# Kernel tuning notes

Hardware: AMD Instinct MI355X
Metric: run time of the kernel (lower is better)

Reference implementation:

```python
import jax, jax.numpy as jnp
import numpy as np

INF = 1000000000000.0
B, H, EMB = 64, 512, 512
V = 32000
S_ENC, S_SEQ = 512, 512
ENC2 = 512  # 2 * encoder_hidden_dim
NUM_OOV = 50


def setup_inputs() -> dict:
    key = jax.random.key(0)
    ks = jax.random.split(key, 24)
    s = 0.02
    nrm = lambda k, shp: jax.random.normal(k, shp, jnp.float32) * s
    inp = {}
    inp["input_ids"] = jax.random.randint(ks[0], (B,), 0, V)
    inp["prev_context"] = jax.random.normal(ks[1], (B, H), jnp.float32)
    inp["h0"] = jax.random.normal(ks[2], (1, B, H), jnp.float32)
    inp["c0"] = jax.random.normal(ks[3], (1, B, H), jnp.float32)
    inp["encoder_outputs"] = jax.random.normal(ks[4], (B, S_ENC, H), jnp.float32)
    inp["seqs_encoding"] = jax.random.normal(ks[5], (B, S_SEQ, ENC2), jnp.float32)
    inp["seqs_encoding_mask"] = jax.random.randint(ks[6], (B, S_SEQ), 0, 2).astype(bool)
    ext = jax.random.randint(ks[7], (B, S_SEQ), 0, V + NUM_OOV)
    inp["ext_idx"] = ext.at[0, 0].set(V + NUM_OOV - 1)  # pin max so num_oov=NUM_OOV
    # parameters (torch Linear convention: y = x @ W.T + b)
    inp["embed"] = nrm(ks[8], (V, EMB))
    inp["W_reduce"] = nrm(ks[9], (EMB, EMB + H)); inp["b_reduce"] = jnp.zeros((EMB,), jnp.float32)
    inp["W_key"] = nrm(ks[10], (H, H)); inp["b_key"] = jnp.zeros((H,), jnp.float32)
    inp["W_comb"] = nrm(ks[11], (H, 2 * H)); inp["b_comb"] = jnp.zeros((H,), jnp.float32)
    inp["W_seqkey"] = nrm(ks[12], (H, ENC2))
    inp["W_ih"] = nrm(ks[13], (4 * H, EMB)); inp["W_hh"] = nrm(ks[14], (4 * H, H))
    inp["b_ih"] = jnp.zeros((4 * H,), jnp.float32); inp["b_hh"] = jnp.zeros((4 * H,), jnp.float32)
    inp["W_out"] = nrm(ks[15], (V, H)); inp["b_out"] = jnp.zeros((V,), jnp.float32)
    return inp


def reference(input_ids, prev_context, h0, c0, encoder_outputs, seqs_encoding,
              seqs_encoding_mask, ext_idx, embed, W_reduce, b_reduce, W_key, b_key,
              W_comb, b_comb, W_seqkey, W_ih, W_hh, b_ih, b_hh, W_out, b_out):
    # embed + (dropout is identity at p=0 / eval) + reduce
    embedded = embed[input_ids]                                   # [B, EMB]
    x = jnp.concatenate([embedded, prev_context], axis=1) @ W_reduce.T + b_reduce  # [B, EMB]
    # single-step, single-layer LSTM (PyTorch gate order i, f, g, o)
    h, c = h0[0], c0[0]
    gates = x @ W_ih.T + b_ih + h @ W_hh.T + b_hh                 # [B, 4H]
    i, f, g, o = jnp.split(gates, 4, axis=-1)
    c1 = jax.nn.sigmoid(f) * c + jax.nn.sigmoid(i) * jnp.tanh(g)
    h1 = jax.nn.sigmoid(o) * jnp.tanh(c1)                         # [B, H]
    output = h1
    # masked attention over encoder_outputs
    enc_mask = encoder_outputs.sum(axis=-1) == 0                  # [B, S_enc]
    keys = encoder_outputs @ W_key.T + b_key                      # [B, S_enc, H]
    energies = jnp.einsum('bsh,bh->bs', keys, output)
    energies = jnp.where(enc_mask, 1e-12, energies)
    attn_weights = jax.nn.softmax(energies, axis=-1)
    context = jnp.einsum('bs,bsh->bh', attn_weights, encoder_outputs)  # [B, H]
    combined = jnp.tanh(jnp.concatenate([output, context], axis=1) @ W_comb.T + b_comb)
    logits = combined @ W_out.T + b_out                           # [B, V]
    # masked attention energies over token sequence for the copy mechanism
    seq_keys = jnp.tanh(seqs_encoding @ W_seqkey.T)               # [B, S_seq, H]
    seq_energies = jnp.einsum('bsh,bh->bs', seq_keys, output)
    seq_energies = jnp.where(seqs_encoding_mask, 1e-12, seq_energies)
    # extended vocab + scatter_max pointer-copy
    extended = jnp.concatenate([logits, jnp.zeros((B, NUM_OOV), logits.dtype)], axis=1)  # [B, V+OOV]
    copy = jnp.full_like(extended, -INF)
    copy = copy.at[jnp.arange(B)[:, None], ext_idx].max(seq_energies)
    copy = jnp.where(copy == -INF, 0.0, copy)
    out = extended + copy
    out = jnp.where(out == 0.0, -INF, out)
    out = jax.nn.log_softmax(out, axis=1)
    return (out, context, h1[None], c1[None], attn_weights)
```

## Files before the change

### kernel.cpp

```cpp
#include <hip/hip_runtime.h>
#include <math.h>

#define B_N    64
#define H_N    512
#define V_N    32000
#define S_N    512
#define VEXT   32050
#define INF_F  1000000000000.0f

typedef __attribute__((ext_vector_type(4))) float floatx4;
typedef __attribute__((ext_vector_type(8))) __bf16 bf16x8;

#define OFF_OUT0 0
#define OFF_CTX  (B_N * VEXT)
#define OFF_H1   (OFF_CTX + B_N * H_N)
#define OFF_C1   (OFF_H1 + B_N * H_N)
#define OFF_ATTN (OFF_C1 + B_N * H_N)

#define WS_FLAG   0
#define WS_X      16
#define WS_GATES  (WS_X + B_N * H_N)
#define WS_Q      (WS_GATES + B_N * 4 * H_N)
#define WS_KB     (WS_Q + B_N * H_N)
#define WS_EN     (WS_KB + B_N)
#define WS_COMB   (WS_EN + B_N * S_N)
#define WS_SEQE   (WS_COMB + B_N * H_N)
#define WS_WSKBF  (WS_SEQE + B_N * S_N)
#define WS_LOGITS (WS_WSKBF + (H_N * H_N) / 2)
#define WS_COPY   (WS_LOGITS + B_N * V_N)
#define WS_RMAX   (WS_COPY + B_N * VEXT)
#define WS_RSUM   (WS_RMAX + B_N)

__device__ __forceinline__ float sigm(float x) { return 1.0f / (1.0f + expf(-x)); }

__device__ __forceinline__ unsigned short f2bf(float f) {
    unsigned u = __float_as_uint(f);
    u += 0x7fffu + ((u >> 16) & 1u);
    return (unsigned short)(u >> 16);
}

__device__ __forceinline__ unsigned enc_f(float f) {
    unsigned u = __float_as_uint(f);
    return (u & 0x80000000u) ? ~u : (u | 0x80000000u);
}
__device__ __forceinline__ float dec_f(unsigned e) {
    unsigned u = (e & 0x80000000u) ? (e & 0x7fffffffu) : ~e;
    return __uint_as_float(u);
}

__global__ void kDetect(const unsigned int* __restrict__ m, int* __restrict__ flag) {
    __shared__ int any;
    if (threadIdx.x == 0) any = 0;
    __syncthreads();
    int loc = 0;
    for (int i = threadIdx.x; i < 8192; i += 256) loc |= (m[i] > 1u) ? 1 : 0;
    if (loc) any = 1;
    __syncthreads();
    if (threadIdx.x == 0) *flag = any;
}

__global__ void kConvertW(const float* __restrict__ W, unsigned short* __restrict__ swz) {
    const int g = blockIdx.x * 256 + threadIdx.x;
    const int t = g >> 10, kc = (g >> 6) & 15, lane = g & 63;
    const int r = t * 16 + (lane & 15);
    const int k = kc * 32 + (lane >> 4) * 8;
    const float4 v0 = *(const float4*)(W + (size_t)r * 512 + k);
    const float4 v1 = *(const float4*)(W + (size_t)r * 512 + k + 4);
    ushort4 h0, h1;
    h0.x = f2bf(v0.x); h0.y = f2bf(v0.y); h0.z = f2bf(v0.z); h0.w = f2bf(v0.w);
    h1.x = f2bf(v1.x); h1.y = f2bf(v1.y); h1.z = f2bf(v1.z); h1.w = f2bf(v1.w);
    *(ushort4*)(swz + (size_t)g * 8) = h0;
    *(ushort4*)(swz + (size_t)g * 8 + 4) = h1;
}

__global__ void kFillCopy(unsigned int* __restrict__ copyenc,
                          unsigned int* __restrict__ rmax, float* __restrict__ rsum) {
    const unsigned NE = enc_f(-INF_F);
    if (blockIdx.x == 0 && threadIdx.x < B_N) {
        rmax[threadIdx.x] = 0u;
        rsum[threadIdx.x] = 0.0f;
    }
    int i0 = (blockIdx.x * 256 + threadIdx.x) * 4;
#pragma unroll
    for (int k = 0; k < 4; k++) {
        int i = i0 + k;
        if (i < B_N * VEXT) copyenc[i] = NE;
    }
}

__global__ __launch_bounds__(256) void kEmbedReduce(
        const int* __restrict__ ids, const float* __restrict__ embed,
        const float* __restrict__ pctx, const float* __restrict__ Wred,
        const float* __restrict__ bred, float* __restrict__ x) {
    __shared__ float xc[1024];
    const int tid = threadIdx.x;
    const int b = blockIdx.x >> 1, half = blockIdx.x & 1;
    const float* er = embed + (size_t)ids[b] * 512;
    xc[tid] = er[tid];               xc[tid + 256] = er[tid + 256];
    xc[512 + tid] = pctx[b * 512 + tid]; xc[512 + tid + 256] = pctx[b * 512 + tid + 256];
    __syncthreads();
    const int j = half * 256 + tid;
    const float4* w4 = (const float4*)(Wred + (size_t)j * 1024);
    const float4* x4 = (const float4*)xc;
    float acc = bred[j];
    for (int k = 0; k < 256; k++) {
        float4 w = w4[k], xv = x4[k];
        acc += w.x * xv.x + w.y * xv.y + w.z * xv.z + w.w * xv.w;
    }
    x[b * 512 + j] = acc;
}

__global__ __launch_bounds__(256) void kGates(
        const float* __restrict__ x, const float* __restrict__ h0,
        const float* __restrict__ Wih, const float* __restrict__ Whh,
        const float* __restrict__ bih, const float* __restrict__ bhh,
        float* __restrict__ gates) {
    __shared__ float xl[512], hl[512];
    const int tid = threadIdx.x;
    const int b = blockIdx.x >> 3, part = blockIdx.x & 7;
    xl[tid] = x[b * 512 + tid];  xl[tid + 256] = x[b * 512 + tid + 256];
    hl[tid] = h0[b * 512 + tid]; hl[tid + 256] = h0[b * 512 + tid + 256];
    __syncthreads();
    const int j = part * 256 + tid;
    const float4* wi4 = (const float4*)(Wih + (size_t)j * 512);
    const float4* wh4 = (const float4*)(Whh + (size_t)j * 512);
    const float4* x4 = (const float4*)xl;
    const float4* h4 = (const float4*)hl;
    float acc = bih[j] + bhh[j];
    for (int k = 0; k < 128; k++) {
        float4 w = wi4[k], xv = x4[k];
        acc += w.x * xv.x + w.y * xv.y + w.z * xv.z + w.w * xv.w;
    }
    for (int k = 0; k < 128; k++) {
        float4 w = wh4[k], hv = h4[k];
        acc += w.x * hv.x + w.y * hv.y + w.z * hv.z + w.w * hv.w;
    }
    gates[(size_t)b * 2048 + j] = acc;
}

__global__ __launch_bounds__(256) void kLstm(
        const float* __restrict__ gates, const float* __restrict__ c0,
        float* __restrict__ h1o, float* __restrict__ c1o) {
    const int idx = blockIdx.x * 256 + threadIdx.x;
    const int b = idx >> 9, j = idx & 511;
    const float gi = gates[(size_t)b * 2048 + j];
    const float gf = gates[(size_t)b * 2048 + 512 + j];
    const float gg = gates[(size_t)b * 2048 + 1024 + j];
    const float go = gates[(size_t)b * 2048 + 1536 + j];
    const float cp = c0[idx];
    const float c1 = sigm(gf) * cp + sigm(gi) * tanhf(gg);
    const float h1 = sigm(go) * tanhf(c1);
    h1o[idx] = h1;
    c1o[idx] = c1;
}

__global__ __launch_bounds__(256) void kQ(
        const float* __restrict__ h1, const float* __restrict__ Wkey,
        const float* __restrict__ bkey, float* __restrict__ q, float* __restrict__ kb) {
    __shared__ float hl[512];
    __shared__ float rd[256];
    const int tid = threadIdx.x;
    const int b = blockIdx.x >> 1, half = blockIdx.x & 1;
    hl[tid] = h1[b * 512 + tid]; hl[tid + 256] = h1[b * 512 + tid + 256];
    __syncthreads();
    const int k = half * 256 + tid;
    float acc = 0.f;
#pragma unroll 4
    for (int h = 0; h < 512; h++) acc += hl[h] * Wkey[(size_t)h * 512 + k];
    q[b * 512 + k] = acc;
    if (half == 0) {
        float p = bkey[tid] * hl[tid] + bkey[tid + 256] * hl[tid + 256];
        rd[tid] = p; __syncthreads();
        for (int st = 128; st > 0; st >>= 1) {
            if (tid < st) rd[tid] += rd[tid + st];
            __syncthreads();
        }
        if (tid == 0) kb[b] = rd[0];
    }
}

__global__ __launch_bounds__(256) void kEnergies(
        const float* __restrict__ enc, const float* __restrict__ q,
        const float* __restrict__ kb, float* __restrict__ energ) {
    __shared__ float ql[512];
    __shared__ float pe[256], ps[256];
    const int tid = threadIdx.x;
    const int b = blockIdx.x >> 2;
    const int sc = (blockIdx.x & 3) * 128;
    ql[tid] = q[b * 512 + tid]; ql[tid + 256] = q[b * 512 + tid + 256];
    __syncthreads();
    const int r = tid & 127, hi = tid >> 7;
    const float4* row4 = (const float4*)(enc + (size_t)(b * 512 + sc + r) * 512 + hi * 256);
    const float4* q4 = (const float4*)(ql + hi * 256);
    float e = 0.f, ssum = 0.f;
#pragma unroll 4
    for (int k = 0; k < 64; k++) {
        float4 ev = row4[k], qv = q4[k];
        e += ev.x * qv.x + ev.y * qv.y + ev.z * qv.z + ev.w * qv.w;
        ssum += ev.x + ev.y + ev.z + ev.w;
    }
    pe[tid] = e; ps[tid] = ssum;
    __syncthreads();
    if (tid < 128) {
        float ee = pe[tid] + pe[tid + 128] + kb[b];
        float sm = ps[tid] + ps[tid + 128];
        if (sm == 0.0f) ee = 1e-12f;
        energ[b * 512 + sc + tid] = ee;
    }
}

__global__ __launch_bounds__(256) void kSoftmax(
        const float* __restrict__ energ, float* __restrict__ attn) {
    __shared__ float el[512];
    __shared__ float rd[256];
    const int tid = threadIdx.x, b = blockIdx.x;
    el[tid] = energ[b * 512 + tid]; el[tid + 256] = energ[b * 512 + tid + 256];
    __syncthreads();
    rd[tid] = fmaxf(el[tid], el[tid + 256]); __syncthreads();
    for (int st = 128; st > 0; st >>= 1) {
        if (tid < st) rd[tid] = fmaxf(rd[tid], rd[tid + st]);
        __syncthreads();
    }
    const float m = rd[0]; __syncthreads();
    float v0 = expf(el[tid] - m), v1 = expf(el[tid + 256] - m);
    rd[tid] = v0 + v1; __syncthreads();
    for (int st = 128; st > 0; st >>= 1) {
        if (tid < st) rd[tid] += rd[tid + st];
        __syncthreads();
    }
    const float inv = 1.0f / rd[0];
    attn[b * 512 + tid] = v0 * inv;
    attn[b * 512 + tid + 256] = v1 * inv;
}

__global__ __launch_bounds__(256) void kContext(
        const float* __restrict__ enc, const float* __restrict__ attn,
        float* __restrict__ ctx) {
    __shared__ float al[64];
    const int tid = threadIdx.x;
    const int b = blockIdx.x >> 3, sc = (blockIdx.x & 7) * 64;
    if (tid < 64) al[tid] = attn[b * 512 + sc + tid];
    __syncthreads();
    float a0 = 0.f, a1 = 0.f;
    for (int s = 0; s < 64; s++) {
        const float* row = enc + (size_t)(b * 512 + sc + s) * 512;
        const float av = al[s];
        a0 += av * row[tid];
        a1 += av * row[tid + 256];
    }
    atomicAdd(&ctx[b * 512 + tid], a0);
    atomicAdd(&ctx[b * 512 + tid + 256], a1);
}

__global__ __launch_bounds__(256) void kCombined(
        const float* __restrict__ h1, const float* __restrict__ ctx,
        const float* __restrict__ Wcomb, const float* __restrict__ bcomb,
        float* __restrict__ comb) {
    __shared__ float hc[1024];
    const int tid = threadIdx.x;
    const int b = blockIdx.x >> 1, half = blockIdx.x & 1;
    hc[tid] = h1[b * 512 + tid];        hc[tid + 256] = h1[b * 512 + tid + 256];
    hc[512 + tid] = ctx[b * 512 + tid]; hc[512 + tid + 256] = ctx[b * 512 + tid + 256];
    __syncthreads();
    const int j = half * 256 + tid;
    const float4* w4 = (const float4*)(Wcomb + (size_t)j * 1024);
    const float4* x4 = (const float4*)hc;
    float acc = bcomb[j];
    for (int k = 0; k < 256; k++) {
        float4 w = w4[k], xv = x4[k];
        acc += w.x * xv.x + w.y * xv.y + w.z * xv.z + w.w * xv.w;
    }
    comb[b * 512 + j] = tanhf(acc);
}

__global__ __launch_bounds__(256) void kLogits(
        const float* __restrict__ comb, const float* __restrict__ Wout,
        const float* __restrict__ bout, float* __restrict__ logits) {
    __shared__ float cl[4][32][64];
    const int tid = threadIdx.x;
    const int vt = tid & 63, kq = tid >> 6;
    const int v = blockIdx.x * 64 + vt;
    float acc[64];
#pragma unroll
    for (int i = 0; i < 64; i++) acc[i] = 0.f;
    for (int kc = 0; kc < 4; kc++) {
        __syncthreads();
        {
            const float4* s4 = (const float4*)(comb + (size_t)vt * 512 + kq * 128 + kc * 32);
#pragma unroll
            for (int qq = 0; qq < 8; qq++) {
                float4 vv = s4[qq];
                cl[kq][qq * 4 + 0][vt] = vv.x; cl[kq][qq * 4 + 1][vt] = vv.y;
                cl[kq][qq * 4 + 2][vt] = vv.z; cl[kq][qq * 4 + 3][vt] = vv.w;
            }
        }
        __syncthreads();
        float wreg[32];
        const float4* w4 = (const float4*)(Wout + (size_t)v * 512 + kq * 128 + kc * 32);
#pragma unroll
        for (int qq = 0; qq < 8; qq++) {
            float4 wv = w4[qq];
            wreg[qq * 4 + 0] = wv.x; wreg[qq * 4 + 1] = wv.y;
            wreg[qq * 4 + 2] = wv.z; wreg[qq * 4 + 3] = wv.w;
        }
#pragma unroll
        for (int kk = 0; kk < 32; kk++) {
            const float wv = wreg[kk];
            const float4* cp = (const float4*)&cl[kq][kk][0];
#pragma unroll
            for (int b4 = 0; b4 < 16; b4++) {
                float4 c4 = cp[b4];
                acc[b4 * 4 + 0] += wv * c4.x; acc[b4 * 4 + 1] += wv * c4.y;
                acc[b4 * 4 + 2] += wv * c4.z; acc[b4 * 4 + 3] += wv * c4.w;
            }
        }
    }
    float* red = &cl[0][0][0];
    __syncthreads();
    if (kq >= 2) {
#pragma unroll
        for (int b = 0; b < 64; b++) red[(kq - 2) * 4096 + vt * 64 + b] = acc[b];
    }
    __syncthreads();
    if (kq < 2) {
#pragma unroll
        for (int b = 0; b < 64; b++) acc[b] += red[kq * 4096 + vt * 64 + b];
    }
    __syncthreads();
    if (kq == 1) {
#pragma unroll
        for (int b = 0; b < 64; b++) red[vt * 64 + b] = acc[b];
    }
    __syncthreads();
    if (kq == 0) {
        const float bo = bout[v];
#pragma unroll
        for (int b = 0; b < 64; b++)
            logits[(size_t)b * 32000 + v] = acc[b] + red[vt * 64 + b] + bo;
    }
}

#define A_STRIDE 520
__global__ __launch_bounds__(512, 4) void kSeqGemm(
        const float* __restrict__ seqs, const unsigned short* __restrict__ swz,
        const float* __restrict__ h1g, float* __restrict__ seq_e) {
    __shared__ unsigned short a_lds[64 * A_STRIDE];
    __shared__ float h1l[512];
    __shared__ float partf[8][64];
    const int tid = threadIdx.x;
    const int m0 = blockIdx.x * 64;
    const int b = m0 >> 9;
    const int w = tid >> 6;
    const int lane = tid & 63;
    const int quad = lane >> 4;
    const int c16 = lane & 15;

    h1l[tid] = h1g[b * 512 + tid];

    {
        const int row = tid >> 3, seg = tid & 7;
        const float* src = seqs + (size_t)(m0 + row) * 512 + seg * 4;
        unsigned short* dst = &a_lds[row * A_STRIDE + seg * 4];
#pragma unroll
        for (int i = 0; i < 16; i++) {
            float4 v = *(const float4*)(src + i * 32);
            ushort4 hv;
            hv.x = f2bf(v.x); hv.y = f2bf(v.y); hv.z = f2bf(v.z); hv.w = f2bf(v.w);
            *(ushort4*)(dst + i * 32) = hv;
        }
    }
    __syncthreads();

    floatx4 acc[4][4];
    const floatx4 zf = {0.f, 0.f, 0.f, 0.f};
#pragma unroll
    for (int i = 0; i < 4; i++)
#pragma unroll
        for (int j = 0; j < 4; j++) acc[i][j] = zf;

    const unsigned short* bbase = swz + (size_t)((w * 4) * 16) * 512 + (size_t)lane * 8;
#pragma unroll 2
    for (int kc = 0; kc < 16; kc++) {
        bf16x8 af[4], bfr[4];
#pragma unroll
        for (int nt = 0; nt < 4; nt++)
            bfr[nt] = *(const bf16x8*)(bbase + (size_t)(nt * 16 + kc) * 512);
#pragma unroll
        for (int ms = 0; ms < 4; ms++)
            af[ms] = *(const bf16x8*)&a_lds[(ms * 16 + c16) * A_STRIDE + kc * 32 + quad * 8];
#pragma unroll
        for (int ms = 0; ms < 4; ms++)
#pragma unroll
            for (int nt = 0; nt < 4; nt++)
                acc[ms][nt] = __builtin_amdgcn_mfma_f32_16x16x32_bf16(
                    af[ms], bfr[nt], acc[ms][nt], 0, 0, 0);
    }

    float psum[16];
#pragma unroll
    for (int i = 0; i < 16; i++) psum[i] = 0.f;
#pragma unroll
    for (int ms = 0; ms < 4; ms++)
#pragma unroll
        for (int nt = 0; nt < 4; nt++) {
            const float hv = h1l[w * 64 + nt * 16 + c16];
#pragma unroll
            for (int r = 0; r < 4; r++)
                psum[ms * 4 + r] += tanhf(acc[ms][nt][r]) * hv;
        }
#pragma unroll
    for (int d = 1; d < 16; d <<= 1)
#pragma unroll
        for (int i = 0; i < 16; i++) psum[i] += __shfl_xor(psum[i], d);
    if (c16 == 0) {
#pragma unroll
        for (int ms = 0; ms < 4; ms++)
#pragma unroll
            for (int r = 0; r < 4; r++)
                partf[w][ms * 16 + quad * 4 + r] = psum[ms * 4 + r];
    }
    __syncthreads();
    if (tid < 64) {
        float s = 0.f;
#pragma unroll
        for (int ww = 0; ww < 8; ww++) s += partf[ww][tid];
        seq_e[m0 + tid] = s;
    }
}

__global__ __launch_bounds__(512) void kScatter(
        const float* __restrict__ seq_e, const void* __restrict__ mask,
        const int* __restrict__ extix, const int* __restrict__ flag,
        unsigned int* __restrict__ copyenc) {
    const int tid = threadIdx.x, b = blockIdx.x;
    float e = seq_e[b * 512 + tid];
    bool mk;
    if (*flag) mk = ((const unsigned char*)mask)[b * 512 + tid] != 0;
    else       mk = ((const int*)mask)[b * 512 + tid] != 0;
    if (mk) e = 1e-12f;
    const int idx = extix[b * 512 + tid];
    atomicMax(&copyenc[(size_t)b * VEXT + idx], enc_f(e));
}

__global__ __launch_bounds__(256) void kFinal1(
        const float* __restrict__ logits, const unsigned int* __restrict__ copyenc,
        float* __restrict__ out0, unsigned int* __restrict__ rmax) {
    __shared__ float rd[4];
    const int tid = threadIdx.x;
    const int b = blockIdx.x >> 4, chunk = blockIdx.x & 15;
    const int base = chunk * 2048 + tid;
    const float* lrow = logits + (size_t)b * 32000;
    const unsigned int* crow = copyenc + (size_t)b * VEXT;
    float* orow = out0 + (size_t)b * VEXT;
    float lm = -3.0e38f;
#pragma unroll
    for (int k = 0; k < 8; k++) {
        const int j = base + k * 256;
        if (j < VEXT) {
            float ext = (j < 32000) ? lrow[j] : 0.0f;
            float cv = dec_f(crow[j]);
            if (cv == -INF_F) cv = 0.0f;
            float o = ext + cv;
            if (o == 0.0f) o = -INF_F;
            orow[j] = o;
            lm = fmaxf(lm, o);
        }
    }
#pragma unroll
    for (int d = 1; d < 64; d <<= 1) lm = fmaxf(lm, __shfl_xor(lm, d));
    if ((tid & 63) == 0) rd[tid >> 6] = lm;
    __syncthreads();
    if (tid == 0) {
        float m = fmaxf(fmaxf(rd[0], rd[1]), fmaxf(rd[2], rd[3]));
        atomicMax(&rmax[b], enc_f(m));
    }
}

__global__ __launch_bounds__(256) void kFinal2(
        const float* __restrict__ out0, const unsigned int* __restrict__ rmax,
        float* __restrict__ rsum) {
    __shared__ float rd[4];
    const int tid = threadIdx.x;
    const int b = blockIdx.x >> 4, chunk = blockIdx.x & 15;
    const int base = chunk * 2048 + tid;
    const float* orow = out0 + (size_t)b * VEXT;
    const float m = dec_f(rmax[b]);
    float s = 0.f;
#pragma unroll
    for (int k = 0; k < 8; k++) {
        const int j = base + k * 256;
        if (j < VEXT) s += expf(orow[j] - m);
    }
#pragma unroll
    for (int d = 1; d < 64; d <<= 1) s += __shfl_xor(s, d);
    if ((tid & 63) == 0) rd[tid >> 6] = s;
    __syncthreads();
    if (tid == 0) atomicAdd(&rsum[b], rd[0] + rd[1] + rd[2] + rd[3]);
}

__global__ __launch_bounds__(256) void kFinal3(
        float* __restrict__ out0, const unsigned int* __restrict__ rmax,
        const float* __restrict__ rsum) {
    const int tid = threadIdx.x;
    const int b = blockIdx.x >> 4, chunk = blockIdx.x & 15;
    const int base = chunk * 2048 + tid;
    float* orow = out0 + (size_t)b * VEXT;
    const float lse = dec_f(rmax[b]) + logf(rsum[b]);
#pragma unroll
    for (int k = 0; k < 8; k++) {
        const int j = base + k * 256;
        if (j < VEXT) orow[j] -= lse;
    }
}

extern "C" void kernel_launch(void* const* d_in, const int* in_sizes, int n_in,
                              void* d_out, int out_size, void* d_ws, size_t ws_size,
                              hipStream_t stream) {
    const int*   ids   = (const int*)d_in[0];
    const float* pctx  = (const float*)d_in[1];
    const float* h0    = (const float*)d_in[2];
    const float* c0    = (const float*)d_in[3];
    const float* enc   = (const float*)d_in[4];
    const float* seqs  = (const float*)d_in[5];
    const void*  mask  = d_in[6];
    const int*   extix = (const int*)d_in[7];
    const float* embed = (const float*)d_in[8];
    const float* Wred  = (const float*)d_in[9];
    const float* bred  = (const float*)d_in[10];
    const float* Wkey  = (const float*)d_in[11];
    const float* bkey  = (const float*)d_in[12];
    const float* Wcomb = (const float*)d_in[13];
    const float* bcomb = (const float*)d_in[14];
    const float* Wseqk = (const float*)d_in[15];
    const float* Wih   = (const float*)d_in[16];
    const float* Whh   = (const float*)d_in[17];
    const float* bih   = (const float*)d_in[18];
    const float* bhh   = (const float*)d_in[19];
    const float* Wout  = (const float*)d_in[20];
    const float* bout  = (const float*)d_in[21];
    (void)in_sizes; (void)n_in; (void)out_size; (void)ws_size;

    float* out = (float*)d_out;
    float* ws = (float*)d_ws;
    int* flag = (int*)ws;
    float* xws = ws + WS_X;
    float* gatesws = ws + WS_GATES;
    float* qws = ws + WS_Q;
    float* kbws = ws + WS_KB;
    float* enws = ws + WS_EN;
    float* combws = ws + WS_COMB;
    float* seqews = ws + WS_SEQE;
    unsigned short* wsk = (unsigned short*)(ws + WS_WSKBF);
    float* logitsws = ws + WS_LOGITS;
    unsigned int* copyenc = (unsigned int*)(ws + WS_COPY);
    unsigned int* rmax = (unsigned int*)(ws + WS_RMAX);
    float* rsum = ws + WS_RSUM;

    kDetect<<<1, 256, 0, stream>>>((const unsigned int*)mask, flag);
    kConvertW<<<128, 256, 0, stream>>>(Wseqk, wsk);
    kFillCopy<<<2004, 256, 0, stream>>>(copyenc, rmax, rsum);
    kEmbedReduce<<<128, 256, 0, stream>>>(ids, embed, pctx, Wred, bred, xws);
    kGates<<<512, 256, 0, stream>>>(xws, h0, Wih, Whh, bih, bhh, gatesws);
    kLstm<<<128, 256, 0, stream>>>(gatesws, c0, out + OFF_H1, out + OFF_C1);
    kQ<<<128, 256, 0, stream>>>(out + OFF_H1, Wkey, bkey, qws, kbws);
    kEnergies<<<256, 256, 0, stream>>>(enc, qws, kbws, enws);
    kSoftmax<<<64, 256, 0, stream>>>(enws, out + OFF_ATTN);
    hipMemsetAsync(out + OFF_CTX, 0, (size_t)B_N * H_N * sizeof(float), stream);
    kContext<<<512, 256, 0, stream>>>(enc, out + OFF_ATTN, out + OFF_CTX);
    kCombined<<<128, 256, 0, stream>>>(out + OFF_H1, out + OFF_CTX, Wcomb, bcomb, combws);
    kLogits<<<500, 256, 0, stream>>>(combws, Wout, bout, logitsws);
    kSeqGemm<<<512, 512, 0, stream>>>(seqs, wsk, out + OFF_H1, seqews);
    kScatter<<<64, 512, 0, stream>>>(seqews, mask, extix, flag, copyenc);
    kFinal1<<<1024, 256, 0, stream>>>(logitsws, copyenc, out + OFF_OUT0, rmax);
    kFinal2<<<1024, 256, 0, stream>>>(out + OFF_OUT0, rmax, rsum);
    kFinal3<<<1024, 256, 0, stream>>>(out + OFF_OUT0, rmax, rsum);
}
```

Measured before the change: 571.7 us.

## Batch small linears across the batch and move logits GEMM to bf16 MFMA

The old per-batch-row GEMV kernels for the reduce, gates and combine linears are replaced with a generic kLin kernel. Each block stages all 64 batch rows of the input in LDS and reuses every weight row across the whole batch, so weights are read once instead of once per batch row. The combine step now writes its tanh output directly as bf16 in an MFMA-fragment-swizzled layout. The logits GEMM becomes a bf16 MFMA kernel that converts W_out tiles to bf16 in LDS, replacing the fp32 scalar FMA loop and its cross-warp reduction. This trades fp32 precision for bf16 inputs on the largest GEMM.

```diff
diff --git a/kernel.cpp b/kernel.cpp
--- a/kernel.cpp
+++ b/kernel.cpp
@@ -88,54 +88,71 @@
     }
 }
 
-__global__ __launch_bounds__(256) void kEmbedReduce(
-        const int* __restrict__ ids, const float* __restrict__ embed,
-        const float* __restrict__ pctx, const float* __restrict__ Wred,
-        const float* __restrict__ bred, float* __restrict__ x) {
-    __shared__ float xc[1024];
-    const int tid = threadIdx.x;
-    const int b = blockIdx.x >> 1, half = blockIdx.x & 1;
-    const float* er = embed + (size_t)ids[b] * 512;
-    xc[tid] = er[tid];               xc[tid + 256] = er[tid + 256];
-    xc[512 + tid] = pctx[b * 512 + tid]; xc[512 + tid + 256] = pctx[b * 512 + tid + 256];
-    __syncthreads();
-    const int j = half * 256 + tid;
-    const float4* w4 = (const float4*)(Wred + (size_t)j * 1024);
-    const float4* x4 = (const float4*)xc;
-    float acc = bred[j];
-    for (int k = 0; k < 256; k++) {
-        float4 w = w4[k], xv = x4[k];
-        acc += w.x * xv.x + w.y * xv.y + w.z * xv.z + w.w * xv.w;
-    }
-    x[b * 512 + j] = acc;
-}
-
-__global__ __launch_bounds__(256) void kGates(
-        const float* __restrict__ x, const float* __restrict__ h0,
-        const float* __restrict__ Wih, const float* __restrict__ Whh,
-        const float* __restrict__ bih, const float* __restrict__ bhh,
-        float* __restrict__ gates) {
-    __shared__ float xl[512], hl[512];
-    const int tid = threadIdx.x;
-    const int b = blockIdx.x >> 3, part = blockIdx.x & 7;
-    xl[tid] = x[b * 512 + tid];  xl[tid + 256] = x[b * 512 + tid + 256];
-    hl[tid] = h0[b * 512 + tid]; hl[tid + 256] = h0[b * 512 + tid + 256];
-    __syncthreads();
-    const int j = part * 256 + tid;
-    const float4* wi4 = (const float4*)(Wih + (size_t)j * 512);
-    const float4* wh4 = (const float4*)(Whh + (size_t)j * 512);
-    const float4* x4 = (const float4*)xl;
-    const float4* h4 = (const float4*)hl;
-    float acc = bih[j] + bhh[j];
-    for (int k = 0; k < 128; k++) {
-        float4 w = wi4[k], xv = x4[k];
-        acc += w.x * xv.x + w.y * xv.y + w.z * xv.z + w.w * xv.w;
-    }
-    for (int k = 0; k < 128; k++) {
-        float4 w = wh4[k], hv = h4[k];
-        acc += w.x * hv.x + w.y * hv.y + w.z * hv.z + w.w * hv.w;
-    }
-    gates[(size_t)b * 2048 + j] = acc;
+__global__ __launch_bounds__(256) void kLin(
+        const float* __restrict__ x0, const int* __restrict__ ids,
+        const float* __restrict__ x1,
+        const float* __restrict__ W0, int ws0,
+        const float* __restrict__ W1, int ws1,
+        const float* __restrict__ b0, const float* __restrict__ b1,
+        int N, int act, float* __restrict__ yout, unsigned short* __restrict__ yswz) {
+    __shared__ float Xl[128 * 65];
+    __shared__ int idsl[64];
+    const int tid = threadIdx.x;
+    const int lane = tid & 63;
+    const int w = __builtin_amdgcn_readfirstlane(tid >> 6);
+    const int j0 = blockIdx.x * 16 + w * 4;
+
+    if (ids && tid < 64) idsl[tid] = ids[tid];
+
+    float acc[4] = {0.f, 0.f, 0.f, 0.f};
+
+    for (int kc = 0; kc < 8; kc++) {
+        __syncthreads();
+#pragma unroll
+        for (int i = 0; i < 8; i++) {
+            const int idx = i * 256 + tid;
+            const int b = idx >> 5, c4 = idx & 31;
+            const float* src = (kc < 4)
+                ? x0 + (size_t)(ids ? idsl[b] : b) * 512 + kc * 128 + c4 * 4
+                : x1 + (size_t)b * 512 + (kc - 4) * 128 + c4 * 4;
+            float4 v = *(const float4*)src;
+            Xl[(c4 * 4 + 0) * 65 + b] = v.x;
+            Xl[(c4 * 4 + 1) * 65 + b] = v.y;
+            Xl[(c4 * 4 + 2) * 65 + b] = v.z;
+            Xl[(c4 * 4 + 3) * 65 + b] = v.w;
+        }
+        __syncthreads();
+        const float* wb[4];
+#pragma unroll
+        for (int jj = 0; jj < 4; jj++)
+            wb[jj] = (kc < 4) ? W0 + (size_t)(j0 + jj) * ws0 + kc * 128
+                              : W1 + (size_t)(j0 + jj) * ws1 + (kc - 4) * 128;
+#pragma unroll 4
+        for (int k4 = 0; k4 < 32; k4++) {
+            const float xv0 = Xl[(k4 * 4 + 0) * 65 + lane];
+            const float xv1 = Xl[(k4 * 4 + 1) * 65 + lane];
+            const float xv2 = Xl[(k4 * 4 + 2) * 65 + lane];
+            const float xv3 = Xl[(k4 * 4 + 3) * 65 + lane];
+#pragma unroll
+            for (int jj = 0; jj < 4; jj++) {
+                const float* wr = wb[jj] + k4 * 4;
+                acc[jj] += xv0 * wr[0] + xv1 * wr[1] + xv2 * wr[2] + xv3 * wr[3];
+            }
+        }
+    }
+#pragma unroll
+    for (int jj = 0; jj < 4; jj++) {
+        const int j = j0 + jj;
+        float val = acc[jj] + b0[j];
+        if (b1) val += b1[j];
+        if (act) val = tanhf(val);
+        if (yout) yout[(size_t)lane * N + j] = val;
+        if (yswz) {
+            const int ms = lane >> 4, c16 = lane & 15;
+            const int kcj = j >> 5, quad = (j >> 3) & 3, q = j & 7;
+            yswz[((size_t)(ms * 16 + kcj) * 64 + quad * 16 + c16) * 8 + q] = f2bf(val);
+        }
+    }
 }
 
 __global__ __launch_bounds__(256) void kLstm(
@@ -252,92 +269,53 @@
     atomicAdd(&ctx[b * 512 + tid + 256], a1);
 }
 
-__global__ __launch_bounds__(256) void kCombined(
-        const float* __restrict__ h1, const float* __restrict__ ctx,
-        const float* __restrict__ Wcomb, const float* __restrict__ bcomb,
-        float* __restrict__ comb) {
-    __shared__ float hc[1024];
-    const int tid = threadIdx.x;
-    const int b = blockIdx.x >> 1, half = blockIdx.x & 1;
-    hc[tid] = h1[b * 512 + tid];        hc[tid + 256] = h1[b * 512 + tid + 256];
-    hc[512 + tid] = ctx[b * 512 + tid]; hc[512 + tid + 256] = ctx[b * 512 + tid + 256];
-    __syncthreads();
-    const int j = half * 256 + tid;
-    const float4* w4 = (const float4*)(Wcomb + (size_t)j * 1024);
-    const float4* x4 = (const float4*)hc;
-    float acc = bcomb[j];
-    for (int k = 0; k < 256; k++) {
-        float4 w = w4[k], xv = x4[k];
-        acc += w.x * xv.x + w.y * xv.y + w.z * xv.z + w.w * xv.w;
-    }
-    comb[b * 512 + j] = tanhf(acc);
-}
-
 __global__ __launch_bounds__(256) void kLogits(
-        const float* __restrict__ comb, const float* __restrict__ Wout,
+        const unsigned short* __restrict__ swzA, const float* __restrict__ Wout,
         const float* __restrict__ bout, float* __restrict__ logits) {
-    __shared__ float cl[4][32][64];
-    const int tid = threadIdx.x;
-    const int vt = tid & 63, kq = tid >> 6;
-    const int v = blockIdx.x * 64 + vt;
-    float acc[64];
-#pragma unroll
-    for (int i = 0; i < 64; i++) acc[i] = 0.f;
-    for (int kc = 0; kc < 4; kc++) {
+    __shared__ unsigned short bl[64 * 144];
+    const int tid = threadIdx.x;
+    const int w = __builtin_amdgcn_readfirstlane(tid >> 6);
+    const int lane = tid & 63;
+    const int quad = lane >> 4, c16 = lane & 15;
+    const int v0 = blockIdx.x * 64;
+
+    floatx4 acc[4];
+    const floatx4 zf = {0.f, 0.f, 0.f, 0.f};
+#pragma unroll
+    for (int i = 0; i < 4; i++) acc[i] = zf;
+
+    for (int c = 0; c < 4; c++) {
         __syncthreads();
-        {
-            const float4* s4 = (const float4*)(comb + (size_t)vt * 512 + kq * 128 + kc * 32);
-#pragma unroll
-            for (int qq = 0; qq < 8; qq++) {
-                float4 vv = s4[qq];
-                cl[kq][qq * 4 + 0][vt] = vv.x; cl[kq][qq * 4 + 1][vt] = vv.y;
-                cl[kq][qq * 4 + 2][vt] = vv.z; cl[kq][qq * 4 + 3][vt] = vv.w;
+#pragma unroll
+        for (int i = 0; i < 8; i++) {
+            const int idx = i * 256 + tid;
+            const int r = idx >> 5, c4 = idx & 31;
+            float4 vv = *(const float4*)(Wout + (size_t)(v0 + r) * 512 + c * 128 + c4 * 4);
+            ushort4 h;
+            h.x = f2bf(vv.x); h.y = f2bf(vv.y); h.z = f2bf(vv.z); h.w = f2bf(vv.w);
+            *(ushort4*)&bl[r * 144 + c4 * 4] = h;
+        }
+        __syncthreads();
+#pragma unroll
+        for (int kl = 0; kl < 4; kl++) {
+            const int kc = c * 4 + kl;
+            const bf16x8 bfrag = *(const bf16x8*)&bl[(w * 16 + c16) * 144 + kl * 32 + quad * 8];
+#pragma unroll
+            for (int ms = 0; ms < 4; ms++) {
+                const bf16x8 afrag = *(const bf16x8*)(swzA + ((size_t)(ms * 16 + kc) * 64 + lane) * 8);
+                acc[ms] = __builtin_amdgcn_mfma_f32_16x16x32_bf16(afrag, bfrag, acc[ms], 0, 0, 0);
             }
         }
-        __syncthreads();
-        float wreg[32];
-        const float4* w4 = (const float4*)(Wout + (size_t)v * 512 + kq * 128 + kc * 32);
-#pragma unroll
-        for (int qq = 0; qq < 8; qq++) {
-            float4 wv = w4[qq];
-            wreg[qq * 4 + 0] = wv.x; wreg[qq * 4 + 1] = wv.y;
-            wreg[qq * 4 + 2] = wv.z; wreg[qq * 4 + 3] = wv.w;
-        }
-#pragma unroll
-        for (int kk = 0; kk < 32; kk++) {
-            const float wv = wreg[kk];
-            const float4* cp = (const float4*)&cl[kq][kk][0];
-#pragma unroll
-            for (int b4 = 0; b4 < 16; b4++) {
-                float4 c4 = cp[b4];
-                acc[b4 * 4 + 0] += wv * c4.x; acc[b4 * 4 + 1] += wv * c4.y;
-                acc[b4 * 4 + 2] += wv * c4.z; acc[b4 * 4 + 3] += wv * c4.w;
-            }
-        }
-    }
-    float* red = &cl[0][0][0];
-    __syncthreads();
-    if (kq >= 2) {
-#pragma unroll
-        for (int b = 0; b < 64; b++) red[(kq - 2) * 4096 + vt * 64 + b] = acc[b];
-    }
-    __syncthreads();
-    if (kq < 2) {
-#pragma unroll
-        for (int b = 0; b < 64; b++) acc[b] += red[kq * 4096 + vt * 64 + b];
-    }
-    __syncthreads();
-    if (kq == 1) {
-#pragma unroll
-        for (int b = 0; b < 64; b++) red[vt * 64 + b] = acc[b];
-    }
-    __syncthreads();
-    if (kq == 0) {
-        const float bo = bout[v];
-#pragma unroll
-        for (int b = 0; b < 64; b++)
-            logits[(size_t)b * 32000 + v] = acc[b] + red[vt * 64 + b] + bo;
-    }
+    }
+    const int v = v0 + w * 16 + c16;
+    const float bo = bout[v];
+#pragma unroll
+    for (int ms = 0; ms < 4; ms++)
+#pragma unroll
+        for (int r = 0; r < 4; r++) {
+            const int b = ms * 16 + quad * 4 + r;
+            logits[(size_t)b * 32000 + v] = acc[ms][r] + bo;
+        }
 }
 
 #define A_STRIDE 520
@@ -548,7 +526,7 @@
     float* qws = ws + WS_Q;
     float* kbws = ws + WS_KB;
     float* enws = ws + WS_EN;
-    float* combws = ws + WS_COMB;
+    unsigned short* combswz = (unsigned short*)(ws + WS_COMB);
     float* seqews = ws + WS_SEQE;
     unsigned short* wsk = (unsigned short*)(ws + WS_WSKBF);
     float* logitsws = ws + WS_LOGITS;
@@ -559,16 +537,20 @@
     kDetect<<<1, 256, 0, stream>>>((const unsigned int*)mask, flag);
     kConvertW<<<128, 256, 0, stream>>>(Wseqk, wsk);
     kFillCopy<<<2004, 256, 0, stream>>>(copyenc, rmax, rsum);
-    kEmbedReduce<<<128, 256, 0, stream>>>(ids, embed, pctx, Wred, bred, xws);
-    kGates<<<512, 256, 0, stream>>>(xws, h0, Wih, Whh, bih, bhh, gatesws);
+    kLin<<<32, 256, 0, stream>>>(embed, ids, pctx, Wred, 1024, Wred + 512, 1024,
+                                 bred, (const float*)nullptr, 512, 0, xws, (unsigned short*)nullptr);
+    kLin<<<128, 256, 0, stream>>>(xws, (const int*)nullptr, h0, Wih, 512, Whh, 512,
+                                  bih, bhh, 2048, 0, gatesws, (unsigned short*)nullptr);
     kLstm<<<128, 256, 0, stream>>>(gatesws, c0, out + OFF_H1, out + OFF_C1);
     kQ<<<128, 256, 0, stream>>>(out + OFF_H1, Wkey, bkey, qws, kbws);
     kEnergies<<<256, 256, 0, stream>>>(enc, qws, kbws, enws);
     kSoftmax<<<64, 256, 0, stream>>>(enws, out + OFF_ATTN);
     hipMemsetAsync(out + OFF_CTX, 0, (size_t)B_N * H_N * sizeof(float), stream);
     kContext<<<512, 256, 0, stream>>>(enc, out + OFF_ATTN, out + OFF_CTX);
-    kCombined<<<128, 256, 0, stream>>>(out + OFF_H1, out + OFF_CTX, Wcomb, bcomb, combws);
-    kLogits<<<500, 256, 0, stream>>>(combws, Wout, bout, logitsws);
+    kLin<<<32, 256, 0, stream>>>(out + OFF_H1, (const int*)nullptr, out + OFF_CTX,
+                                 Wcomb, 1024, Wcomb + 512, 1024, bcomb,
+                                 (const float*)nullptr, 512, 1, (float*)nullptr, combswz);
+    kLogits<<<500, 256, 0, stream>>>(combswz, Wout, bout, logitsws);
     kSeqGemm<<<512, 512, 0, stream>>>(seqs, wsk, out + OFF_H1, seqews);
     kScatter<<<64, 512, 0, stream>>>(seqews, mask, extix, flag, copyenc);
     kFinal1<<<1024, 256, 0, stream>>>(logitsws, copyenc, out + OFF_OUT0, rmax);
```

New measurement: 694.7 us. 1.22x slower.
